# Kernel tuning notes

Hardware: AMD Instinct MI355X
Metric: run time of the kernel (lower is better)

The kernel has to match this reference:

```python
import jax, jax.numpy as jnp
from jax import lax
import numpy as np

KH, KW = 7, 7


def setup_inputs() -> dict:
    key = jax.random.key(0)
    kx, _ = jax.random.split(key)
    x = jax.random.uniform(kx, (32, 3, 1024, 1024), dtype=jnp.float32)
    # Box kernel of ones; normalization (normalized=True) happens in reference.
    kernel = jnp.ones((KH, KW), dtype=jnp.float32)
    return {"x": x, "kernel": kernel}


def reference(x, kernel):
    # BoxBlur: normalized box kernel, reflect padding, depthwise 2D conv.
    kh, kw = kernel.shape
    k = kernel / jnp.sum(kernel)  # L1-normalized box kernel (normalized=True)
    # reflect padding by k//2 on each spatial side (kornia compute_padding for odd k)
    xp = jnp.pad(x, ((0, 0), (0, 0), (kh // 2, kh // 2), (kw // 2, kw // 2)), mode="reflect")
    C = x.shape[1]
    w = jnp.broadcast_to(k[None, None], (C, 1, kh, kw))  # depthwise: one kernel per channel
    out = lax.conv_general_dilated(
        xp, w,
        window_strides=(1, 1),
        padding="VALID",
        dimension_numbers=("NCHW", "OIHW", "NCHW"),
        feature_group_count=C,
    )
    return out
```

## Files before the change

### kernel.cpp

```cpp
#include <hip/hip_runtime.h>

#define TH 64
#define ITERS 16

__device__ __forceinline__ int reflect_idx(int i, int n) {
    if (i < 0) i = -i;
    if (i >= n) i = 2 * n - 2 - i;
    return i;
}

__device__ __forceinline__ float4 ld4(const float* p) {
    return *reinterpret_cast<const float4*>(p);
}

struct Row3 { float4 A, B, C; };

__device__ __forceinline__ Row3 load_row3(const float* __restrict__ row, int x0, int W,
                                          bool xlo, bool xhi) {
    Row3 r;
    r.B = ld4(row + x0);
    const float* pa = row + (xlo ? x0 : x0 - 4);
    const float* pc = row + (xhi ? x0 : x0 + 4);
    r.A = ld4(pa);
    r.C = ld4(pc);
    if (xlo) r.A = make_float4(r.C.x, r.B.w, r.B.z, r.B.y);
    if (xhi) r.C = make_float4(r.B.z, r.B.y, r.B.x, r.A.w);
    return r;
}

__device__ __forceinline__ float4 hsum(const Row3& t) {
    float h0 = t.A.y + t.A.z + t.A.w + t.B.x + t.B.y + t.B.z + t.B.w;
    float h1 = h0 - t.A.y + t.C.x;
    float h2 = h1 - t.A.z + t.C.y;
    float h3 = h2 - t.A.w + t.C.z;
    return make_float4(h0, h1, h2, h3);
}

__global__ __launch_bounds__(256) void boxblur_kernel(const float* __restrict__ in,
                                                      float* __restrict__ out,
                                                      int H, int W, int cpx) {
    const int bid = blockIdx.x;
    const int sbid = (bid & 7) * cpx + (bid >> 3);
    const int plane = sbid >> 4;
    const int y0 = (sbid & 15) * TH;

    const float* __restrict__ src = in + (size_t)plane * H * W;
    float* __restrict__ dst = out + (size_t)plane * H * W;

    const int x0 = threadIdx.x * 4;
    const bool xlo = (x0 == 0), xhi = (x0 + 4 == W);

    float4 w[10];
#pragma unroll
    for (int j = 0; j < 6; ++j) {
        const float* rp = src + (size_t)reflect_idx(y0 - 3 + j, H) * W;
        w[j] = hsum(load_row3(rp, x0, W, xlo, xhi));
    }
    Row3 n0 = load_row3(src + (size_t)reflect_idx(y0 + 3, H) * W, x0, W, xlo, xhi);
    Row3 n1 = load_row3(src + (size_t)reflect_idx(y0 + 4, H) * W, x0, W, xlo, xhi);
    Row3 n2 = load_row3(src + (size_t)reflect_idx(y0 + 5, H) * W, x0, W, xlo, xhi);
    Row3 n3 = load_row3(src + (size_t)reflect_idx(y0 + 6, H) * W, x0, W, xlo, xhi);

    const float inv = 1.0f / 49.0f;
    float* orow = dst + (size_t)y0 * W + x0;

#pragma unroll
    for (int t = 0; t < ITERS; ++t) {
        w[6] = hsum(n0);
        w[7] = hsum(n1);
        w[8] = hsum(n2);
        w[9] = hsum(n3);

        if (t < ITERS - 1) {
            const int yb = y0 + 4 * t + 7;
            n0 = load_row3(src + (size_t)reflect_idx(yb + 0, H) * W, x0, W, xlo, xhi);
            n1 = load_row3(src + (size_t)reflect_idx(yb + 1, H) * W, x0, W, xlo, xhi);
            n2 = load_row3(src + (size_t)reflect_idx(yb + 2, H) * W, x0, W, xlo, xhi);
            n3 = load_row3(src + (size_t)reflect_idx(yb + 3, H) * W, x0, W, xlo, xhi);
        }

        float4 vs = make_float4(
            w[0].x + w[1].x + w[2].x + w[3].x + w[4].x + w[5].x + w[6].x,
            w[0].y + w[1].y + w[2].y + w[3].y + w[4].y + w[5].y + w[6].y,
            w[0].z + w[1].z + w[2].z + w[3].z + w[4].z + w[5].z + w[6].z,
            w[0].w + w[1].w + w[2].w + w[3].w + w[4].w + w[5].w + w[6].w);
        *reinterpret_cast<float4*>(orow) =
            make_float4(vs.x * inv, vs.y * inv, vs.z * inv, vs.w * inv);
        vs.x += w[7].x - w[0].x; vs.y += w[7].y - w[0].y;
        vs.z += w[7].z - w[0].z; vs.w += w[7].w - w[0].w;
        *reinterpret_cast<float4*>(orow + W) =
            make_float4(vs.x * inv, vs.y * inv, vs.z * inv, vs.w * inv);
        vs.x += w[8].x - w[1].x; vs.y += w[8].y - w[1].y;
        vs.z += w[8].z - w[1].z; vs.w += w[8].w - w[1].w;
        *reinterpret_cast<float4*>(orow + 2 * W) =
            make_float4(vs.x * inv, vs.y * inv, vs.z * inv, vs.w * inv);
        vs.x += w[9].x - w[2].x; vs.y += w[9].y - w[2].y;
        vs.z += w[9].z - w[2].z; vs.w += w[9].w - w[2].w;
        *reinterpret_cast<float4*>(orow + 3 * W) =
            make_float4(vs.x * inv, vs.y * inv, vs.z * inv, vs.w * inv);
        orow += 4 * W;

        w[0] = w[4]; w[1] = w[5]; w[2] = w[6];
        w[3] = w[7]; w[4] = w[8]; w[5] = w[9];
    }
}

extern "C" void kernel_launch(void* const* d_in, const int* in_sizes, int n_in,
                              void* d_out, int out_size, void* d_ws, size_t ws_size,
                              hipStream_t stream) {
    const float* x = (const float*)d_in[0];
    float* out = (float*)d_out;
    const int H = 1024, W = 1024;
    const int NC = 32 * 3;
    const int nwg = NC * (H / TH);
    dim3 grid(nwg);
    dim3 block(256);
    boxblur_kernel<<<grid, block, 0, stream>>>(x, out, H, W, nwg / 8);
}
```

Before: 178.5 us.

## Restructure box blur into deep 8-row load pipeline with nontemporal stores

Each block now covers 128 rows instead of 64, halving the halo re-reads. The inner loop is rebuilt as an 8-stage software pipeline: eight row loads stay in flight, and a running vertical sum is updated one row at a time through a ring of horizontal sums. Reflect fixups move from load time to consumption time so loads can issue earlier, and outputs use nontemporal stores. Launch bounds now request 3 waves per SIMD. In exchange it holds more registers, and the final loads run past the tile, possibly into reflected rows that are never used.

```diff
diff --git a/kernel.cpp b/kernel.cpp
--- a/kernel.cpp
+++ b/kernel.cpp
@@ -1,7 +1,9 @@
 #include <hip/hip_runtime.h>
 
-#define TH 64
-#define ITERS 16
+#define BH 128
+#define NB 8
+
+typedef float f32x4 __attribute__((ext_vector_type(4)));
 
 __device__ __forceinline__ int reflect_idx(int i, int n) {
     if (i < 0) i = -i;
@@ -15,7 +17,7 @@
 
 struct Row3 { float4 A, B, C; };
 
-__device__ __forceinline__ Row3 load_row3(const float* __restrict__ row, int x0, int W,
+__device__ __forceinline__ Row3 load_row3(const float* __restrict__ row, int x0,
                                           bool xlo, bool xhi) {
     Row3 r;
     r.B = ld4(row + x0);
@@ -23,12 +25,12 @@
     const float* pc = row + (xhi ? x0 : x0 + 4);
     r.A = ld4(pa);
     r.C = ld4(pc);
-    if (xlo) r.A = make_float4(r.C.x, r.B.w, r.B.z, r.B.y);
-    if (xhi) r.C = make_float4(r.B.z, r.B.y, r.B.x, r.A.w);
     return r;
 }
 
-__device__ __forceinline__ float4 hsum(const Row3& t) {
+__device__ __forceinline__ float4 hsum_fix(Row3 t, bool xlo, bool xhi) {
+    if (xlo) t.A = make_float4(t.C.x, t.B.w, t.B.z, t.B.y);
+    if (xhi) t.C = make_float4(t.B.z, t.B.y, t.B.x, t.A.w);
     float h0 = t.A.y + t.A.z + t.A.w + t.B.x + t.B.y + t.B.z + t.B.w;
     float h1 = h0 - t.A.y + t.C.x;
     float h2 = h1 - t.A.z + t.C.y;
@@ -36,13 +38,13 @@
     return make_float4(h0, h1, h2, h3);
 }
 
-__global__ __launch_bounds__(256) void boxblur_kernel(const float* __restrict__ in,
-                                                      float* __restrict__ out,
-                                                      int H, int W, int cpx) {
+__global__ __launch_bounds__(256, 3) void boxblur_kernel(const float* __restrict__ in,
+                                                         float* __restrict__ out,
+                                                         int H, int W, int cpx) {
     const int bid = blockIdx.x;
     const int sbid = (bid & 7) * cpx + (bid >> 3);
-    const int plane = sbid >> 4;
-    const int y0 = (sbid & 15) * TH;
+    const int plane = sbid >> 3;
+    const int y0 = (sbid & 7) * BH;
 
     const float* __restrict__ src = in + (size_t)plane * H * W;
     float* __restrict__ dst = out + (size_t)plane * H * W;
@@ -50,59 +52,47 @@
     const int x0 = threadIdx.x * 4;
     const bool xlo = (x0 == 0), xhi = (x0 + 4 == W);
 
-    float4 w[10];
+    float4 hr[8];
+    float4 vs = make_float4(0.f, 0.f, 0.f, 0.f);
 #pragma unroll
-    for (int j = 0; j < 6; ++j) {
-        const float* rp = src + (size_t)reflect_idx(y0 - 3 + j, H) * W;
-        w[j] = hsum(load_row3(rp, x0, W, xlo, xhi));
+    for (int j = 0; j < 7; ++j) {
+        const float* rp = src + (size_t)reflect_idx(y0 - 4 + j, H) * W;
+        float4 h = hsum_fix(load_row3(rp, x0, xlo, xhi), xlo, xhi);
+        hr[1 + j] = h;
+        vs.x += h.x; vs.y += h.y; vs.z += h.z; vs.w += h.w;
     }
-    Row3 n0 = load_row3(src + (size_t)reflect_idx(y0 + 3, H) * W, x0, W, xlo, xhi);
-    Row3 n1 = load_row3(src + (size_t)reflect_idx(y0 + 4, H) * W, x0, W, xlo, xhi);
-    Row3 n2 = load_row3(src + (size_t)reflect_idx(y0 + 5, H) * W, x0, W, xlo, xhi);
-    Row3 n3 = load_row3(src + (size_t)reflect_idx(y0 + 6, H) * W, x0, W, xlo, xhi);
+
+    Row3 s0 = load_row3(src + (size_t)reflect_idx(y0 + 3, H) * W, x0, xlo, xhi);
+    Row3 s1 = load_row3(src + (size_t)reflect_idx(y0 + 4, H) * W, x0, xlo, xhi);
+    Row3 s2 = load_row3(src + (size_t)reflect_idx(y0 + 5, H) * W, x0, xlo, xhi);
+    Row3 s3 = load_row3(src + (size_t)reflect_idx(y0 + 6, H) * W, x0, xlo, xhi);
+    Row3 s4 = load_row3(src + (size_t)reflect_idx(y0 + 7, H) * W, x0, xlo, xhi);
+    Row3 s5 = load_row3(src + (size_t)reflect_idx(y0 + 8, H) * W, x0, xlo, xhi);
+    Row3 s6 = load_row3(src + (size_t)reflect_idx(y0 + 9, H) * W, x0, xlo, xhi);
+    Row3 s7 = load_row3(src + (size_t)reflect_idx(y0 + 10, H) * W, x0, xlo, xhi);
 
     const float inv = 1.0f / 49.0f;
     float* orow = dst + (size_t)y0 * W + x0;
+    int yload = y0 + 11;
 
-#pragma unroll
-    for (int t = 0; t < ITERS; ++t) {
-        w[6] = hsum(n0);
-        w[7] = hsum(n1);
-        w[8] = hsum(n2);
-        w[9] = hsum(n3);
+#define PHASE(p, pn)                                                              \
+    {                                                                             \
+        float4 hn = hsum_fix(s##p, xlo, xhi);                                     \
+        vs.x += hn.x - hr[pn].x; vs.y += hn.y - hr[pn].y;                         \
+        vs.z += hn.z - hr[pn].z; vs.w += hn.w - hr[pn].w;                         \
+        hr[p] = hn;                                                               \
+        f32x4 o = { vs.x * inv, vs.y * inv, vs.z * inv, vs.w * inv };             \
+        __builtin_nontemporal_store(o, reinterpret_cast<f32x4*>(orow));           \
+        orow += W;                                                                \
+        s##p = load_row3(src + (size_t)reflect_idx(yload, H) * W, x0, xlo, xhi);  \
+        ++yload;                                                                  \
+    }
 
-        if (t < ITERS - 1) {
-            const int yb = y0 + 4 * t + 7;
-            n0 = load_row3(src + (size_t)reflect_idx(yb + 0, H) * W, x0, W, xlo, xhi);
-            n1 = load_row3(src + (size_t)reflect_idx(yb + 1, H) * W, x0, W, xlo, xhi);
-            n2 = load_row3(src + (size_t)reflect_idx(yb + 2, H) * W, x0, W, xlo, xhi);
-            n3 = load_row3(src + (size_t)reflect_idx(yb + 3, H) * W, x0, W, xlo, xhi);
-        }
-
-        float4 vs = make_float4(
-            w[0].x + w[1].x + w[2].x + w[3].x + w[4].x + w[5].x + w[6].x,
-            w[0].y + w[1].y + w[2].y + w[3].y + w[4].y + w[5].y + w[6].y,
-            w[0].z + w[1].z + w[2].z + w[3].z + w[4].z + w[5].z + w[6].z,
-            w[0].w + w[1].w + w[2].w + w[3].w + w[4].w + w[5].w + w[6].w);
-        *reinterpret_cast<float4*>(orow) =
-            make_float4(vs.x * inv, vs.y * inv, vs.z * inv, vs.w * inv);
-        vs.x += w[7].x - w[0].x; vs.y += w[7].y - w[0].y;
-        vs.z += w[7].z - w[0].z; vs.w += w[7].w - w[0].w;
-        *reinterpret_cast<float4*>(orow + W) =
-            make_float4(vs.x * inv, vs.y * inv, vs.z * inv, vs.w * inv);
-        vs.x += w[8].x - w[1].x; vs.y += w[8].y - w[1].y;
-        vs.z += w[8].z - w[1].z; vs.w += w[8].w - w[1].w;
-        *reinterpret_cast<float4*>(orow + 2 * W) =
-            make_float4(vs.x * inv, vs.y * inv, vs.z * inv, vs.w * inv);
-        vs.x += w[9].x - w[2].x; vs.y += w[9].y - w[2].y;
-        vs.z += w[9].z - w[2].z; vs.w += w[9].w - w[2].w;
-        *reinterpret_cast<float4*>(orow + 3 * W) =
-            make_float4(vs.x * inv, vs.y * inv, vs.z * inv, vs.w * inv);
-        orow += 4 * W;
-
-        w[0] = w[4]; w[1] = w[5]; w[2] = w[6];
-        w[3] = w[7]; w[4] = w[8]; w[5] = w[9];
+    for (int it = 0; it < BH / 8; ++it) {
+        PHASE(0, 1) PHASE(1, 2) PHASE(2, 3) PHASE(3, 4)
+        PHASE(4, 5) PHASE(5, 6) PHASE(6, 7) PHASE(7, 0)
     }
+#undef PHASE
 }
 
 extern "C" void kernel_launch(void* const* d_in, const int* in_sizes, int n_in,
@@ -112,7 +102,7 @@
     float* out = (float*)d_out;
     const int H = 1024, W = 1024;
     const int NC = 32 * 3;
-    const int nwg = NC * (H / TH);
+    const int nwg = NC * NB;
     dim3 grid(nwg);
     dim3 block(256);
     boxblur_kernel<<<grid, block, 0, stream>>>(x, out, H, W, nwg / 8);
```

After: 176.2 us. About the same (-1.3%).
